# Performance work log

Measured on AMD Instinct MI355X. Metric: run time of the kernel, lower is better.

The kernel has to match this reference:

```python
import jax, jax.numpy as jnp
import numpy as np

WS = 7          # window size
SIZE = 56       # spatial H = W
SHIFT = 3       # shift_size = window_size // 2 (mask branch active)
NH = 4          # num heads
EPS = 1e-5


def _rel_pos_index(ws=WS):
    coords = np.stack(np.meshgrid(np.arange(ws), np.arange(ws), indexing='ij'))  # [2,ws,ws]
    coords = coords.reshape(2, -1)                               # [2, ws*ws]
    rel = coords[:, :, None] - coords[:, None, :]                # [2, N, N]
    rel = rel.transpose(1, 2, 0)                                 # [N, N, 2]
    rel[:, :, 0] += ws - 1
    rel[:, :, 1] += ws - 1
    rel[:, :, 0] *= 2 * ws - 1
    return jnp.asarray(rel[:, :, 0] + rel[:, :, 1])              # [N, N] int


def _attn_mask(size=SIZE, ws=WS, shift=SHIFT):
    img = np.zeros((size, size), dtype=np.float32)
    slices = (slice(0, -ws), slice(-ws, -shift), slice(-shift, None))
    cnt = 0
    for h in slices:
        for w in slices:
            img[h, w] = cnt
            cnt += 1
    nw = size // ws
    win = img.reshape(nw, ws, nw, ws).transpose(0, 2, 1, 3).reshape(-1, ws * ws)  # [nW, N]
    diff = win[:, None, :] - win[:, :, None]                    # [nW, N, N]
    mask = np.where(diff != 0, -100.0, 0.0).astype(np.float32)
    return jnp.asarray(mask)


def _layernorm(x, w, b):
    mu = jnp.mean(x, axis=-1, keepdims=True)
    var = jnp.mean(jnp.square(x - mu), axis=-1, keepdims=True)
    return (x - mu) * jax.lax.rsqrt(var + EPS) * w + b


def setup_inputs() -> dict:
    key = jax.random.key(0)
    ks = jax.random.split(key, 8)
    dim, dff = 128, 512
    s = lambda fan: 1.0 / np.sqrt(fan)
    return {
        'x': jax.random.normal(ks[0], (32, SIZE * SIZE, dim), jnp.float32),
        'qkv_w': jax.random.normal(ks[1], (dim, 3 * dim), jnp.float32) * s(dim),
        'qkv_b': jnp.zeros((3 * dim,), jnp.float32),
        'proj_w': jax.random.normal(ks[2], (dim, dim), jnp.float32) * s(dim),
        'proj_b': jnp.zeros((dim,), jnp.float32),
        'rpb_table': jax.random.normal(ks[3], ((2 * WS - 1) ** 2, NH), jnp.float32) * 0.02,
        'ln1_w': jnp.ones((dim,), jnp.float32),
        'ln1_b': jnp.zeros((dim,), jnp.float32),
        'ln2_w': jnp.ones((dim,), jnp.float32),
        'ln2_b': jnp.zeros((dim,), jnp.float32),
        'mlp_w1': jax.random.normal(ks[4], (dim, dff), jnp.float32) * s(dim),
        'mlp_b1': jnp.zeros((dff,), jnp.float32),
        'mlp_w2': jax.random.normal(ks[5], (dff, dim), jnp.float32) * s(dff),
        'mlp_b2': jnp.zeros((dim,), jnp.float32),
    }


def reference(x, qkv_w, qkv_b, proj_w, proj_b, rpb_table,
              ln1_w, ln1_b, ln2_w, ln2_b, mlp_w1, mlp_b1, mlp_w2, mlp_b2):
    B, L, C = x.shape
    N = WS * WS
    nw = SIZE // WS
    nW = nw * nw
    hd = C // NH
    scale = hd ** -0.5

    shortcut = x
    h = _layernorm(x, ln1_w, ln1_b).reshape(B, SIZE, SIZE, C)
    # window partition -> [B*nW, N, C]
    h = h.reshape(B, nw, WS, nw, WS, C).transpose(0, 1, 3, 2, 4, 5).reshape(B * nW, N, C)

    qkv = (h @ qkv_w + qkv_b).reshape(B * nW, N, 3, NH, hd)
    q, k, v = jnp.moveaxis(qkv, 2, 0)                 # each [B*nW, N, NH, hd]
    attn = jnp.einsum('bnhd,bmhd->bhnm', q * scale, k)  # [B*nW, NH, N, N]

    bias = rpb_table[_rel_pos_index()]                # [N, N, NH]
    attn = attn + bias.transpose(2, 0, 1)[None]

    mask = _attn_mask()                               # [nW, N, N]
    attn = attn.reshape(B, nW, NH, N, N) + mask[None, :, None]
    attn = jax.nn.softmax(attn.reshape(B * nW, NH, N, N), axis=-1)

    h = jnp.einsum('bhnm,bmhd->bnhd', attn, v).reshape(B * nW, N, C)
    h = h @ proj_w + proj_b

    # window reverse -> [B, L, C]
    h = h.reshape(B, nw, nw, WS, WS, C).transpose(0, 1, 3, 2, 4, 5).reshape(B, L, C)
    x = shortcut + h

    m = _layernorm(x, ln2_w, ln2_b)
    m = jax.nn.gelu(m @ mlp_w1 + mlp_b1, approximate=False) @ mlp_w2 + mlp_b2
    return x + m
```

## Files before the change

kernel.cpp:

```cpp
#include <hip/hip_runtime.h>
#include <hip/hip_bf16.h>

#define T_TOK   100352
#define NWIN    2048
#define EPS_LN  1e-5f

typedef __attribute__((ext_vector_type(8))) short bf16x8;
typedef __attribute__((ext_vector_type(4))) float f32x4;

__device__ inline float bf2f(unsigned short u) {
  union { unsigned int i; float f; } c; c.i = ((unsigned int)u) << 16; return c.f;
}
__device__ inline unsigned short f2bf(float f) {
  union { float f; unsigned int i; } c; c.f = f;
  unsigned int x = c.i;
  x += 0x7fffu + ((x >> 16) & 1u);
  return (unsigned short)(x >> 16);
}
__device__ inline bf16x8 ld8(const unsigned short* p) {
  return *reinterpret_cast<const bf16x8*>(p);
}

__device__ inline int win_row_to_token(int r) {
  int win = r / 49, n = r % 49;
  int b  = win >> 6, w2 = win & 63;
  int wi = w2 >> 3,  wj = w2 & 7;
  int rr = n / 7,    cc = n % 7;
  return b * 3136 + (wi * 7 + rr) * 56 + (wj * 7 + cc);
}

__global__ void prep_weights(const float* __restrict__ qkv_w,
                             const float* __restrict__ proj_w,
                             const float* __restrict__ w1,
                             const float* __restrict__ w2,
                             unsigned short* __restrict__ wts) {
  int i = blockIdx.x * 256 + threadIdx.x;
  unsigned short* qkvt  = wts;
  unsigned short* projt = wts + 49152;
  unsigned short* w1t   = wts + 65536;
  unsigned short* w2t   = wts + 131072;
  if (i < 49152) {
    int n = i >> 7, k = i & 127; qkvt[i] = f2bf(qkv_w[k * 384 + n]);
  } else if (i < 65536) {
    int e = i - 49152; int n = e >> 7, k = e & 127; projt[e] = f2bf(proj_w[k * 128 + n]);
  } else if (i < 131072) {
    int e = i - 65536; int n = e >> 7, k = e & 127; w1t[e] = f2bf(w1[k * 512 + n]);
  } else if (i < 196608) {
    int e = i - 131072; int n = e >> 9, k = e & 511; w2t[e] = f2bf(w2[k * 128 + n]);
  }
}

__global__ void prep_cls(const float* __restrict__ rpb, float* __restrict__ cls2) {
  int i = blockIdx.x * 256 + threadIdx.x;
  int reg = i & 3, lane = (i >> 2) & 63, ct = (i >> 8) & 3, rt = (i >> 10) & 3,
      h = (i >> 12) & 3, cl = (i >> 14) & 3;
  int n = rt * 16 + ((lane >> 4) << 2) + reg;
  int m = ct * 16 + (lane & 15);
  float v = -30000.f;
  if (n < 49 && m < 49) {
    int nr = n / 7, nc = n % 7, mr = m / 7, mc = m % 7;
    v = rpb[((nr - mr + 6) * 13 + (nc - mc + 6)) * 4 + h];
    int regn = ((cl & 2) ? (nr < 4 ? 3 : 6) : 0) + ((cl & 1) ? (nc < 4 ? 1 : 2) : 0);
    int regm = ((cl & 2) ? (mr < 4 ? 3 : 6) : 0) + ((cl & 1) ? (mc < 4 ? 1 : 2) : 0);
    if (regn != regm) v -= 100.f;
  }
  cls2[i] = v;
}

template<bool WINMAP>
__global__ __launch_bounds__(256) void ln_kernel(const float* __restrict__ x,
                                                 const float* __restrict__ w,
                                                 const float* __restrict__ b,
                                                 unsigned short* __restrict__ out) {
  int r    = blockIdx.x * 4 + (threadIdx.x >> 6);
  int lane = threadIdx.x & 63;
  int src  = WINMAP ? win_row_to_token(r) : r;
  float2 v = *reinterpret_cast<const float2*>(x + (long)src * 128 + lane * 2);
  float s  = v.x + v.y;
  float s2 = v.x * v.x + v.y * v.y;
#pragma unroll
  for (int off = 32; off; off >>= 1) {
    s  += __shfl_xor(s,  off);
    s2 += __shfl_xor(s2, off);
  }
  float mu  = s * (1.f / 128.f);
  float var = s2 * (1.f / 128.f) - mu * mu;
  float inv = rsqrtf(var + EPS_LN);
  int c = lane * 2;
  float2 wv = *reinterpret_cast<const float2*>(w + c);
  float2 bv = *reinterpret_cast<const float2*>(b + c);
  float y0 = (v.x - mu) * inv * wv.x + bv.x;
  float y1 = (v.y - mu) * inv * wv.y + bv.y;
  unsigned int pk = ((unsigned int)f2bf(y1) << 16) | (unsigned int)f2bf(y0);
  *reinterpret_cast<unsigned int*>(out + (long)r * 128 + c) = pk;
}

template<int EPI, int KSTEPS, int NBN>
__global__ __launch_bounds__(256) void gemm_k(const unsigned short* __restrict__ A,
                                              const unsigned short* __restrict__ Wt,
                                              const float* __restrict__ bias,
                                              void* __restrict__ out,
                                              const float* __restrict__ res) {
  const int K = KSTEPS * 32;
  int flat  = blockIdx.x;
  int chunk = gridDim.x >> 3;
  int swz   = (flat & 7) * chunk + (flat >> 3);
  int ntile = swz % NBN, mpan = swz / NBN;

  int lane = threadIdx.x & 63;
  int wid  = threadIdx.x >> 6;
  int rowBase = mpan * 128 + wid * 32;
  int colBase = ntile * 64;
  int m  = lane & 15;
  int kg = lane >> 4;
  f32x4 acc[2][4] = {};
  const unsigned short* Ap = A  + (long)(rowBase + m) * K + kg * 8;
  const unsigned short* Bp = Wt + (long)(colBase + m) * K + kg * 8;
#pragma unroll 4
  for (int ks = 0; ks < KSTEPS; ks++) {
    bf16x8 b0 = ld8(Bp + 0 * 16 * K + ks * 32);
    bf16x8 b1 = ld8(Bp + 1 * 16 * K + ks * 32);
    bf16x8 b2 = ld8(Bp + 2 * 16 * K + ks * 32);
    bf16x8 b3 = ld8(Bp + 3 * 16 * K + ks * 32);
    bf16x8 a0 = ld8(Ap + ks * 32);
    bf16x8 a1 = ld8(Ap + (long)16 * K + ks * 32);
    acc[0][0] = __builtin_amdgcn_mfma_f32_16x16x32_bf16(a0, b0, acc[0][0], 0, 0, 0);
    acc[0][1] = __builtin_amdgcn_mfma_f32_16x16x32_bf16(a0, b1, acc[0][1], 0, 0, 0);
    acc[0][2] = __builtin_amdgcn_mfma_f32_16x16x32_bf16(a0, b2, acc[0][2], 0, 0, 0);
    acc[0][3] = __builtin_amdgcn_mfma_f32_16x16x32_bf16(a0, b3, acc[0][3], 0, 0, 0);
    acc[1][0] = __builtin_amdgcn_mfma_f32_16x16x32_bf16(a1, b0, acc[1][0], 0, 0, 0);
    acc[1][1] = __builtin_amdgcn_mfma_f32_16x16x32_bf16(a1, b1, acc[1][1], 0, 0, 0);
    acc[1][2] = __builtin_amdgcn_mfma_f32_16x16x32_bf16(a1, b2, acc[1][2], 0, 0, 0);
    acc[1][3] = __builtin_amdgcn_mfma_f32_16x16x32_bf16(a1, b3, acc[1][3], 0, 0, 0);
  }
#pragma unroll
  for (int mt = 0; mt < 2; mt++) {
#pragma unroll
    for (int rgi = 0; rgi < 4; rgi++) {
      int row = rowBase + mt * 16 + kg * 4 + rgi;
      int t = (EPI == 1) ? win_row_to_token(row) : row;
#pragma unroll
      for (int j = 0; j < 4; j++) {
        int col = colBase + j * 16 + m;
        float v = acc[mt][j][rgi] + bias[col];
        if (EPI == 0) {
          ((unsigned short*)out)[(long)row * 384 + col] = f2bf(v);
        } else if (EPI == 1) {
          ((float*)out)[(long)t * 128 + col] = res[(long)t * 128 + col] + v;
        } else if (EPI == 2) {
          float u = v * (1.0f + 0.044715f * v * v);
          float g = v / (1.0f + __expf(-1.5957691216f * u));
          ((unsigned short*)out)[(long)row * 512 + col] = f2bf(g);
        } else {
          ((float*)out)[(long)row * 128 + col] = res[(long)row * 128 + col] + v;
        }
      }
    }
  }
}

__global__ __launch_bounds__(256) void attn_mfma(const unsigned short* __restrict__ qkv,
                                                 const float* __restrict__ cls2,
                                                 unsigned short* __restrict__ out) {
  __shared__ unsigned short vt[128 * 64];
  __shared__ unsigned short pb[4][64 * 64];
  int win = blockIdx.x;
  int tid = threadIdx.x;
  const unsigned short* qbase = qkv + (long)win * 49 * 384;

  for (int i = tid; i < 49 * 128; i += 256) {
    int mm = i >> 7, d = i & 127;
    vt[d * 64 + (mm ^ ((d & 7) << 3))] = qbase[mm * 384 + 256 + d];
  }
  for (int i = tid; i < 128 * 15; i += 256) {
    int d = i / 15, mm = 49 + i % 15;
    vt[d * 64 + (mm ^ ((d & 7) << 3))] = 0;
  }

  int h = tid >> 6, lane = tid & 63;
  int lr = lane & 15, g = lane >> 4;
  int w2 = win & 63;
  int cl = (((w2 >> 3) == 7) ? 2 : 0) + (((w2 & 7) == 7) ? 1 : 0);

  bf16x8 aq[4], bk[4];
  bf16x8 zf = {};
#pragma unroll
  for (int rt = 0; rt < 4; rt++)
    aq[rt] = ld8(qbase + (rt * 16 + lr) * 384 + h * 32 + g * 8);
#pragma unroll
  for (int ct = 0; ct < 4; ct++) {
    int mm = ct * 16 + lr;
    bk[ct] = (mm < 49) ? ld8(qbase + mm * 384 + 128 + h * 32 + g * 8) : zf;
  }
  f32x4 acc[4][4] = {};
#pragma unroll
  for (int rt = 0; rt < 4; rt++)
#pragma unroll
    for (int ct = 0; ct < 4; ct++)
      acc[rt][ct] = __builtin_amdgcn_mfma_f32_16x16x32_bf16(aq[rt], bk[ct], acc[rt][ct], 0, 0, 0);

  const float scale = 0.17677669529663687f;
  const float* cb = cls2 + (long)(cl * 4 + h) * 16 * 256;
  unsigned short* P = pb[h];
#pragma unroll
  for (int rt = 0; rt < 4; rt++) {
    f32x4 c[4];
#pragma unroll
    for (int ct = 0; ct < 4; ct++)
      c[ct] = *reinterpret_cast<const f32x4*>(cb + (rt * 4 + ct) * 256 + lane * 4);
#pragma unroll
    for (int reg = 0; reg < 4; reg++) {
      float s0 = acc[rt][0][reg] * scale + c[0][reg];
      float s1 = acc[rt][1][reg] * scale + c[1][reg];
      float s2 = acc[rt][2][reg] * scale + c[2][reg];
      float s3 = acc[rt][3][reg] * scale + c[3][reg];
      float mx = fmaxf(fmaxf(s0, s1), fmaxf(s2, s3));
      mx = fmaxf(mx, __shfl_xor(mx, 1)); mx = fmaxf(mx, __shfl_xor(mx, 2));
      mx = fmaxf(mx, __shfl_xor(mx, 4)); mx = fmaxf(mx, __shfl_xor(mx, 8));
      float p0 = __expf(s0 - mx), p1 = __expf(s1 - mx);
      float p2 = __expf(s2 - mx), p3 = __expf(s3 - mx);
      float sum = p0 + p1 + p2 + p3;
      sum += __shfl_xor(sum, 1); sum += __shfl_xor(sum, 2);
      sum += __shfl_xor(sum, 4); sum += __shfl_xor(sum, 8);
      float inv = 1.f / sum;
      int n = rt * 16 + g * 4 + reg;
      int sw = (n & 7) << 3, rowb = n * 64;
      P[rowb + ((0 * 16 + lr) ^ sw)] = f2bf(p0 * inv);
      P[rowb + ((1 * 16 + lr) ^ sw)] = f2bf(p1 * inv);
      P[rowb + ((2 * 16 + lr) ^ sw)] = f2bf(p2 * inv);
      P[rowb + ((3 * 16 + lr) ^ sw)] = f2bf(p3 * inv);
    }
  }
  __syncthreads();

  f32x4 o[4][2] = {};
  bf16x8 bv[2][2];
#pragma unroll
  for (int dt = 0; dt < 2; dt++)
#pragma unroll
    for (int ks = 0; ks < 2; ks++) {
      int d = h * 32 + dt * 16 + lr;
      bv[dt][ks] = ld8(&vt[d * 64 + ((ks * 32 + g * 8) ^ ((d & 7) << 3))]);
    }
#pragma unroll
  for (int rt = 0; rt < 4; rt++)
#pragma unroll
    for (int ks = 0; ks < 2; ks++) {
      int n = rt * 16 + lr;
      bf16x8 ap = ld8(&P[n * 64 + ((ks * 32 + g * 8) ^ ((n & 7) << 3))]);
#pragma unroll
      for (int dt = 0; dt < 2; dt++)
        o[rt][dt] = __builtin_amdgcn_mfma_f32_16x16x32_bf16(ap, bv[dt][ks], o[rt][dt], 0, 0, 0);
    }
#pragma unroll
  for (int rt = 0; rt < 4; rt++)
#pragma unroll
    for (int dt = 0; dt < 2; dt++)
#pragma unroll
      for (int reg = 0; reg < 4; reg++) {
        int n = rt * 16 + g * 4 + reg;
        if (n < 49)
          out[((long)win * 49 + n) * 128 + h * 32 + dt * 16 + lr] = f2bf(o[rt][dt][reg]);
      }
}

extern "C" void kernel_launch(void* const* d_in, const int* in_sizes, int n_in,
                              void* d_out, int out_size, void* d_ws, size_t ws_size,
                              hipStream_t stream) {
  (void)in_sizes; (void)n_in; (void)out_size; (void)ws_size;
  const float* x      = (const float*)d_in[0];
  const float* qkv_w  = (const float*)d_in[1];
  const float* qkv_b  = (const float*)d_in[2];
  const float* proj_w = (const float*)d_in[3];
  const float* proj_b = (const float*)d_in[4];
  const float* rpb    = (const float*)d_in[5];
  const float* ln1_w  = (const float*)d_in[6];
  const float* ln1_b  = (const float*)d_in[7];
  const float* ln2_w  = (const float*)d_in[8];
  const float* ln2_b  = (const float*)d_in[9];
  const float* w1     = (const float*)d_in[10];
  const float* b1     = (const float*)d_in[11];
  const float* w2     = (const float*)d_in[12];
  const float* b2     = (const float*)d_in[13];

  char* ws = (char*)d_ws;
  unsigned short* wts   = (unsigned short*)ws;
  unsigned short* hb    = (unsigned short*)(ws + 393216);
  unsigned short* qkv   = (unsigned short*)(ws + 26083328);
  unsigned short* attno = hb;
  unsigned short* g     = hb;
  float*          out1  = (float*)(ws + 103153664);
  unsigned short* mbuf  = (unsigned short*)(ws + 154533888);
  float*          cls2  = (float*)(ws + 154533888);

  const int MP = T_TOK / 128;

  prep_weights<<<768, 256, 0, stream>>>(qkv_w, proj_w, w1, w2, wts);
  prep_cls<<<256, 256, 0, stream>>>(rpb, cls2);
  ln_kernel<true><<<T_TOK / 4, 256, 0, stream>>>(x, ln1_w, ln1_b, hb);
  gemm_k<0, 4, 6><<<MP * 6, 256, 0, stream>>>(hb, wts, qkv_b, qkv, nullptr);
  attn_mfma<<<NWIN, 256, 0, stream>>>(qkv, cls2, attno);
  gemm_k<1, 4, 2><<<MP * 2, 256, 0, stream>>>(attno, wts + 49152, proj_b, out1, x);
  ln_kernel<false><<<T_TOK / 4, 256, 0, stream>>>(out1, ln2_w, ln2_b, mbuf);
  gemm_k<2, 4, 8><<<MP * 8, 256, 0, stream>>>(mbuf, wts + 65536, b1, g, nullptr);
  gemm_k<3, 16, 2><<<MP * 2, 256, 0, stream>>>(g, wts + 131072, b2, (float*)d_out, out1);
}
```

Before: 336.7 us.

## Fuse LayerNorm2, MLP fc1+GELU and fc2 into one kernel

Measured after the change: 279.4 us. 17.0% less time.

```diff
diff --git a/kernel.cpp b/kernel.cpp
--- a/kernel.cpp
+++ b/kernel.cpp
@@ -8,9 +8,6 @@
 typedef __attribute__((ext_vector_type(8))) short bf16x8;
 typedef __attribute__((ext_vector_type(4))) float f32x4;
 
-__device__ inline float bf2f(unsigned short u) {
-  union { unsigned int i; float f; } c; c.i = ((unsigned int)u) << 16; return c.f;
-}
 __device__ inline unsigned short f2bf(float f) {
   union { float f; unsigned int i; } c; c.f = f;
   unsigned int x = c.i;
@@ -145,14 +142,8 @@
         float v = acc[mt][j][rgi] + bias[col];
         if (EPI == 0) {
           ((unsigned short*)out)[(long)row * 384 + col] = f2bf(v);
-        } else if (EPI == 1) {
+        } else {
           ((float*)out)[(long)t * 128 + col] = res[(long)t * 128 + col] + v;
-        } else if (EPI == 2) {
-          float u = v * (1.0f + 0.044715f * v * v);
-          float g = v / (1.0f + __expf(-1.5957691216f * u));
-          ((unsigned short*)out)[(long)row * 512 + col] = f2bf(g);
-        } else {
-          ((float*)out)[(long)row * 128 + col] = res[(long)row * 128 + col] + v;
         }
       }
     }
@@ -264,6 +255,99 @@
       }
 }
 
+__global__ __launch_bounds__(512, 1) void mlp_fused(
+    const float* __restrict__ out1,
+    const unsigned short* __restrict__ w1t,
+    const float* __restrict__ b1,
+    const unsigned short* __restrict__ w2t,
+    const float* __restrict__ b2,
+    const float* __restrict__ ln2w,
+    const float* __restrict__ ln2b,
+    float* __restrict__ dout) {
+  __shared__ unsigned short lnm[64 * 136];
+  __shared__ unsigned short gel[64 * 520];
+  long rowbase = (long)blockIdx.x * 64;
+  int tid = threadIdx.x, w = tid >> 6, lane = tid & 63, lr = lane & 15, g = lane >> 4;
+
+  {
+    int c = lane * 2;
+    float2 wv = *(const float2*)(ln2w + c);
+    float2 bv = *(const float2*)(ln2b + c);
+    for (int n = w; n < 64; n += 8) {
+      float2 v = *(const float2*)(out1 + (rowbase + n) * 128 + c);
+      float s = v.x + v.y, s2 = v.x * v.x + v.y * v.y;
+#pragma unroll
+      for (int off = 32; off; off >>= 1) { s += __shfl_xor(s, off); s2 += __shfl_xor(s2, off); }
+      float mu  = s * (1.f / 128.f);
+      float inv = rsqrtf(s2 * (1.f / 128.f) - mu * mu + EPS_LN);
+      float y0 = (v.x - mu) * inv * wv.x + bv.x;
+      float y1 = (v.y - mu) * inv * wv.y + bv.y;
+      unsigned int pk = ((unsigned int)f2bf(y1) << 16) | f2bf(y0);
+      *(unsigned int*)(lnm + n * 136 + c) = pk;
+    }
+  }
+  __syncthreads();
+
+  f32x4 acc[4][4] = {};
+#pragma unroll
+  for (int ksi = 0; ksi < 4; ksi++) {
+    int kof = ksi * 32 + g * 8;
+    bf16x8 av[4], bv[4];
+#pragma unroll
+    for (int rt = 0; rt < 4; rt++)
+      av[rt] = ld8(lnm + (rt * 16 + lr) * 136 + kof);
+#pragma unroll
+    for (int ct = 0; ct < 4; ct++) {
+      int colc = w * 64 + ct * 16 + lr;
+      bv[ct] = ld8(w1t + colc * 128 + kof);
+    }
+#pragma unroll
+    for (int rt = 0; rt < 4; rt++)
+#pragma unroll
+      for (int ct = 0; ct < 4; ct++)
+        acc[rt][ct] = __builtin_amdgcn_mfma_f32_16x16x32_bf16(av[rt], bv[ct], acc[rt][ct], 0, 0, 0);
+  }
+#pragma unroll
+  for (int ct = 0; ct < 4; ct++) {
+    int c = w * 64 + ct * 16 + lr;
+    float bc = b1[c];
+#pragma unroll
+    for (int rt = 0; rt < 4; rt++)
+#pragma unroll
+      for (int rgi = 0; rgi < 4; rgi++) {
+        int n = rt * 16 + g * 4 + rgi;
+        float v = acc[rt][ct][rgi] + bc;
+        float u = v * (1.0f + 0.044715f * v * v);
+        float gv = v / (1.0f + __expf(-1.5957691216f * u));
+        gel[n * 520 + c] = f2bf(gv);
+      }
+  }
+  __syncthreads();
+
+  f32x4 a2[4] = {};
+#pragma unroll 4
+  for (int ksi = 0; ksi < 16; ksi++) {
+    int kof = ksi * 32 + g * 8;
+    bf16x8 aa[4];
+#pragma unroll
+    for (int rt = 0; rt < 4; rt++)
+      aa[rt] = ld8(gel + (rt * 16 + lr) * 520 + kof);
+    bf16x8 bb = ld8(w2t + (w * 16 + lr) * 512 + kof);
+#pragma unroll
+    for (int rt = 0; rt < 4; rt++)
+      a2[rt] = __builtin_amdgcn_mfma_f32_16x16x32_bf16(aa[rt], bb, a2[rt], 0, 0, 0);
+  }
+  int col = w * 16 + lr;
+  float bc2 = b2[col];
+#pragma unroll
+  for (int rt = 0; rt < 4; rt++)
+#pragma unroll
+    for (int rgi = 0; rgi < 4; rgi++) {
+      long row = rowbase + rt * 16 + g * 4 + rgi;
+      dout[row * 128 + col] = out1[row * 128 + col] + bc2 + a2[rt][rgi];
+    }
+}
+
 extern "C" void kernel_launch(void* const* d_in, const int* in_sizes, int n_in,
                               void* d_out, int out_size, void* d_ws, size_t ws_size,
                               hipStream_t stream) {
@@ -288,9 +372,7 @@
   unsigned short* hb    = (unsigned short*)(ws + 393216);
   unsigned short* qkv   = (unsigned short*)(ws + 26083328);
   unsigned short* attno = hb;
-  unsigned short* g     = hb;
   float*          out1  = (float*)(ws + 103153664);
-  unsigned short* mbuf  = (unsigned short*)(ws + 154533888);
   float*          cls2  = (float*)(ws + 154533888);
 
   const int MP = T_TOK / 128;
@@ -301,7 +383,6 @@
   gemm_k<0, 4, 6><<<MP * 6, 256, 0, stream>>>(hb, wts, qkv_b, qkv, nullptr);
   attn_mfma<<<NWIN, 256, 0, stream>>>(qkv, cls2, attno);
   gemm_k<1, 4, 2><<<MP * 2, 256, 0, stream>>>(attno, wts + 49152, proj_b, out1, x);
-  ln_kernel<false><<<T_TOK / 4, 256, 0, stream>>>(out1, ln2_w, ln2_b, mbuf);
-  gemm_k<2, 4, 8><<<MP * 8, 256, 0, stream>>>(mbuf, wts + 65536, b1, g, nullptr);
-  gemm_k<3, 16, 2><<<MP * 2, 256, 0, stream>>>(g, wts + 131072, b2, (float*)d_out, out1);
-}
+  mlp_fused<<<T_TOK / 64, 512, 0, stream>>>(out1, wts + 65536, b1, wts + 131072, b2,
+                                            ln2_w, ln2_b, (float*)d_out);
+}
```

## Fuse LN2, MLP fc1+GELU and fc2 into one per-wave kernel

Applied to the files above, without the earlier changes.

Measured after the change: 405.0 us. 20.3% more time.

```diff
diff --git a/kernel.cpp b/kernel.cpp
--- a/kernel.cpp
+++ b/kernel.cpp
@@ -8,9 +8,6 @@
 typedef __attribute__((ext_vector_type(8))) short bf16x8;
 typedef __attribute__((ext_vector_type(4))) float f32x4;
 
-__device__ inline float bf2f(unsigned short u) {
-  union { unsigned int i; float f; } c; c.i = ((unsigned int)u) << 16; return c.f;
-}
 __device__ inline unsigned short f2bf(float f) {
   union { float f; unsigned int i; } c; c.f = f;
   unsigned int x = c.i;
@@ -145,14 +142,8 @@
         float v = acc[mt][j][rgi] + bias[col];
         if (EPI == 0) {
           ((unsigned short*)out)[(long)row * 384 + col] = f2bf(v);
-        } else if (EPI == 1) {
+        } else {
           ((float*)out)[(long)t * 128 + col] = res[(long)t * 128 + col] + v;
-        } else if (EPI == 2) {
-          float u = v * (1.0f + 0.044715f * v * v);
-          float g = v / (1.0f + __expf(-1.5957691216f * u));
-          ((unsigned short*)out)[(long)row * 512 + col] = f2bf(g);
-        } else {
-          ((float*)out)[(long)row * 128 + col] = res[(long)row * 128 + col] + v;
         }
       }
     }
@@ -264,6 +255,121 @@
       }
 }
 
+__global__ __launch_bounds__(256) void mlp_wave(
+    const float* __restrict__ out1,
+    const unsigned short* __restrict__ w1t,
+    const float* __restrict__ b1,
+    const unsigned short* __restrict__ w2t,
+    const float* __restrict__ b2,
+    const float* __restrict__ ln2w,
+    const float* __restrict__ ln2b,
+    float* __restrict__ dout) {
+  int tid = threadIdx.x, w = tid >> 6, lane = tid & 63, lr = lane & 15, g = lane >> 4;
+  long tok0 = (long)blockIdx.x * 64 + w * 16;
+  const float* xrow = out1 + (tok0 + lr) * 128;
+
+  float xv[32];
+  float s = 0.f, s2 = 0.f;
+#pragma unroll
+  for (int ksi = 0; ksi < 4; ksi++) {
+    f32x4 v0 = *(const f32x4*)(xrow + ksi * 32 + g * 8);
+    f32x4 v1 = *(const f32x4*)(xrow + ksi * 32 + g * 8 + 4);
+#pragma unroll
+    for (int j = 0; j < 4; j++) {
+      xv[ksi * 8 + j]     = v0[j];
+      xv[ksi * 8 + 4 + j] = v1[j];
+      s  += v0[j] + v1[j];
+      s2 += v0[j] * v0[j] + v1[j] * v1[j];
+    }
+  }
+  s  += __shfl_xor(s, 16);  s  += __shfl_xor(s, 32);
+  s2 += __shfl_xor(s2, 16); s2 += __shfl_xor(s2, 32);
+  float mu  = s * (1.f / 128.f);
+  float inv = rsqrtf(s2 * (1.f / 128.f) - mu * mu + EPS_LN);
+
+  bf16x8 aln[4];
+#pragma unroll
+  for (int ksi = 0; ksi < 4; ksi++) {
+    f32x4 w0 = *(const f32x4*)(ln2w + ksi * 32 + g * 8);
+    f32x4 w1v = *(const f32x4*)(ln2w + ksi * 32 + g * 8 + 4);
+    f32x4 c0 = *(const f32x4*)(ln2b + ksi * 32 + g * 8);
+    f32x4 c1 = *(const f32x4*)(ln2b + ksi * 32 + g * 8 + 4);
+    union { unsigned int u[4]; bf16x8 v; } U;
+#pragma unroll
+    for (int d = 0; d < 4; d++) {
+      int j0 = 2 * d, j1 = 2 * d + 1;
+      float wj0 = (j0 < 4) ? w0[j0] : w1v[j0 - 4];
+      float wj1 = (j1 < 4) ? w0[j1] : w1v[j1 - 4];
+      float bj0 = (j0 < 4) ? c0[j0] : c1[j0 - 4];
+      float bj1 = (j1 < 4) ? c0[j1] : c1[j1 - 4];
+      float e0 = (xv[ksi * 8 + j0] - mu) * inv * wj0 + bj0;
+      float e1 = (xv[ksi * 8 + j1] - mu) * inv * wj1 + bj1;
+      U.u[d] = ((unsigned int)f2bf(e1) << 16) | (unsigned int)f2bf(e0);
+    }
+    aln[ksi] = U.v;
+  }
+
+  int idx0 = lr + ((lane & 16) << 1);
+  int idx1 = idx0 + 16;
+  bool hi = (lane & 32) != 0;
+
+  f32x4 d2[8] = {};
+  for (int c = 0; c < 4; c++) {
+    unsigned int pk[8][2];
+#pragma unroll
+    for (int rt = 0; rt < 8; rt++) {
+      f32x4 d1 = {};
+#pragma unroll
+      for (int ksi = 0; ksi < 4; ksi++) {
+        bf16x8 aw = ld8(w1t + (long)(c * 128 + rt * 16 + lr) * 128 + ksi * 32 + g * 8);
+        d1 = __builtin_amdgcn_mfma_f32_16x16x32_bf16(aw, aln[ksi], d1, 0, 0, 0);
+      }
+      f32x4 bb = *(const f32x4*)(b1 + c * 128 + rt * 16 + g * 4);
+      float ge[4];
+#pragma unroll
+      for (int r = 0; r < 4; r++) {
+        float v = d1[r] + bb[r];
+        float u = v * (1.0f + 0.044715f * v * v);
+        ge[r] = v / (1.0f + __expf(-1.5957691216f * u));
+      }
+      pk[rt][0] = ((unsigned int)f2bf(ge[1]) << 16) | (unsigned int)f2bf(ge[0]);
+      pk[rt][1] = ((unsigned int)f2bf(ge[3]) << 16) | (unsigned int)f2bf(ge[2]);
+    }
+#pragma unroll
+    for (int kb = 0; kb < 4; kb++) {
+      unsigned int a0 = __shfl(pk[2 * kb][0], idx0);
+      unsigned int a1 = __shfl(pk[2 * kb][1], idx0);
+      unsigned int a2 = __shfl(pk[2 * kb][0], idx1);
+      unsigned int a3 = __shfl(pk[2 * kb][1], idx1);
+      unsigned int e0 = __shfl(pk[2 * kb + 1][0], idx0);
+      unsigned int e1 = __shfl(pk[2 * kb + 1][1], idx0);
+      unsigned int e2 = __shfl(pk[2 * kb + 1][0], idx1);
+      unsigned int e3 = __shfl(pk[2 * kb + 1][1], idx1);
+      union { unsigned int u[4]; bf16x8 v; } U;
+      U.u[0] = hi ? e0 : a0;
+      U.u[1] = hi ? e1 : a1;
+      U.u[2] = hi ? e2 : a2;
+      U.u[3] = hi ? e3 : a3;
+      bf16x8 bg = U.v;
+#pragma unroll
+      for (int ot = 0; ot < 8; ot++) {
+        bf16x8 aw2 = ld8(w2t + (long)(ot * 16 + lr) * 512 + c * 128 + kb * 32 + g * 8);
+        d2[ot] = __builtin_amdgcn_mfma_f32_16x16x32_bf16(aw2, bg, d2[ot], 0, 0, 0);
+      }
+    }
+  }
+
+#pragma unroll
+  for (int ot = 0; ot < 8; ot++) {
+    f32x4 res = *(const f32x4*)(out1 + (tok0 + lr) * 128 + ot * 16 + g * 4);
+    f32x4 bb2 = *(const f32x4*)(b2 + ot * 16 + g * 4);
+    f32x4 o;
+#pragma unroll
+    for (int r = 0; r < 4; r++) o[r] = res[r] + bb2[r] + d2[ot][r];
+    *(f32x4*)(dout + (tok0 + lr) * 128 + ot * 16 + g * 4) = o;
+  }
+}
+
 extern "C" void kernel_launch(void* const* d_in, const int* in_sizes, int n_in,
                               void* d_out, int out_size, void* d_ws, size_t ws_size,
                               hipStream_t stream) {
@@ -288,9 +394,7 @@
   unsigned short* hb    = (unsigned short*)(ws + 393216);
   unsigned short* qkv   = (unsigned short*)(ws + 26083328);
   unsigned short* attno = hb;
-  unsigned short* g     = hb;
   float*          out1  = (float*)(ws + 103153664);
-  unsigned short* mbuf  = (unsigned short*)(ws + 154533888);
   float*          cls2  = (float*)(ws + 154533888);
 
   const int MP = T_TOK / 128;
@@ -301,7 +405,6 @@
   gemm_k<0, 4, 6><<<MP * 6, 256, 0, stream>>>(hb, wts, qkv_b, qkv, nullptr);
   attn_mfma<<<NWIN, 256, 0, stream>>>(qkv, cls2, attno);
   gemm_k<1, 4, 2><<<MP * 2, 256, 0, stream>>>(attno, wts + 49152, proj_b, out1, x);
-  ln_kernel<false><<<T_TOK / 4, 256, 0, stream>>>(out1, ln2_w, ln2_b, mbuf);
-  gemm_k<2, 4, 8><<<MP * 8, 256, 0, stream>>>(mbuf, wts + 65536, b1, g, nullptr);
-  gemm_k<3, 16, 2><<<MP * 2, 256, 0, stream>>>(g, wts + 131072, b2, (float*)d_out, out1);
-}
+  mlp_wave<<<T_TOK / 64, 256, 0, stream>>>(out1, wts + 65536, b1, wts + 131072, b2,
+                                           ln2_w, ln2_b, (float*)d_out);
+}
```
